# Kernel tuning notes

Hardware: AMD Instinct MI355X
Metric: run time of the kernel (lower is better)

Reference implementation:

```python
import jax, jax.numpy as jnp
import numpy as np

N_MOTIF_PER_CLASS = 8
N_CLASS = 16
N_MOTIF = N_MOTIF_PER_CLASS * N_CLASS
TEMPERATURE = 0.2
TAU = 0.99
K2 = 32
EPS = 1e-4


def setup_inputs() -> dict:
    key = jax.random.key(0)
    k1, k2, k3 = jax.random.split(key, 3)
    N, H = 32768, 1024
    z = jax.random.normal(k1, (N, H), dtype=jnp.float32)
    Motif_Vector = jax.random.normal(k2, (N_MOTIF, H), dtype=jnp.float32)
    y = jax.random.randint(k3, (N,), 0, N_CLASS, dtype=jnp.int64)
    return {"z": z, "Motif_Vector": Motif_Vector, "y": y}


def euclidean_1(X, M):
    # squared euclidean distance via GEMM, then log-ratio similarity
    xp = X @ M.T                                     # [N, n_motif]
    distance = (-2.0 * xp
                + jnp.sum(X * X, axis=1, keepdims=True)
                + jnp.sum(M * M, axis=1)[None, :])
    similarity = jnp.log((distance + 1.0) / (distance + EPS))
    return similarity, distance


def reference(z, Motif_Vector, y):
    similarity, distance = euclidean_1(z, Motif_Vector)

    # mapping: motif j belongs to class j // n_motif_per_class
    motif_class = jnp.arange(N_MOTIF) // N_MOTIF_PER_CLASS   # [n_motif]
    true_motifs = (y[:, None] == motif_class[None, :])       # [N, n_motif]

    # contrastive loss (exact torch math: exp(sim/T), max over positives,
    # sum over negatives)
    sims = jnp.exp(similarity / TEMPERATURE)
    sim_pos = jnp.max(jnp.where(true_motifs, sims, -jnp.inf), axis=1)
    sim_neg_sum = jnp.sum(jnp.where(true_motifs, 0.0, sims), axis=1)
    loss = -jnp.mean(jnp.log(sim_pos / (sim_neg_sum + sim_pos)))

    # update_motif (update_type='topk', weighted_mean=False):
    # torch passes `distance` into filter_similar_graph and argsorts
    # descending, i.e. selects the K2 LARGEST distances among same-class
    # samples (faithful to source).
    masked = jnp.where(true_motifs.T, distance.T, -jnp.inf)  # [n_motif, N]
    _, idx = jax.lax.top_k(masked, K2)                       # [n_motif, K2]
    selected = z[idx]                                        # [n_motif, K2, H]
    new_motif = jnp.mean(selected, axis=1)                   # weights = 1/K2
    new_M = TAU * Motif_Vector + (1.0 - TAU) * new_motif

    return loss, new_M
```

## Files before the change

kernel.cpp:

```cpp
#include <hip/hip_runtime.h>
#include <cstdint>
#include <cmath>

#define NROWS 32768
#define HD    1024
#define NMOT  128
#define NCLS  16
#define KSEL  32
#define EPSV  1e-4f

typedef __attribute__((ext_vector_type(4))) float  f32x4;
typedef __attribute__((ext_vector_type(8))) __bf16 bf16x8;
typedef __attribute__((ext_vector_type(4))) __bf16 bf16x4;
typedef unsigned long long u64;

#define WS_LP   0
#define WS_S1K  1024
#define WS_CD   132096
#define CAPC    256

static __device__ __forceinline__ float dot4(float4 v) {
    return v.x * v.x + v.y * v.y + v.z * v.z + v.w * v.w;
}

static __device__ __forceinline__ bf16x4 cvt4(float4 v) {
    bf16x4 t;
    t[0] = (__bf16)v.x; t[1] = (__bf16)v.y; t[2] = (__bf16)v.z; t[3] = (__bf16)v.w;
    return t;
}

static __device__ __forceinline__ bf16x8 cvt8(float4 a, float4 b) {
    bf16x8 t;
    t[0] = (__bf16)a.x; t[1] = (__bf16)a.y; t[2] = (__bf16)a.z; t[3] = (__bf16)a.w;
    t[4] = (__bf16)b.x; t[5] = (__bf16)b.y; t[6] = (__bf16)b.z; t[7] = (__bf16)b.w;
    return t;
}

static __device__ __forceinline__ u64 pack_key(float v, int idx) {
    unsigned int b = __float_as_uint(v);
    unsigned int mo = (b & 0x80000000u) ? ~b : (b | 0x80000000u);
    unsigned int khi = ~mo;
    return ((u64)khi << 32) | (unsigned int)idx;
}

#define BM 64
#define BN 128
#define BK 32
#define NS (HD / BK)
#define SA 40

__global__ __launch_bounds__(256, 2) void gemm_fused(
    const float* __restrict__ z, const float* __restrict__ mv,
    float* __restrict__ cd, const int* __restrict__ y,
    float* __restrict__ lossP) {
    __shared__ __bf16 As[2][BM * SA];
    __shared__ __bf16 Bs[2][BN * SA];
    __shared__ float  szn[BM];
    __shared__ float  smn[BN];
    __shared__ int    ly[BM];
    __shared__ float  spm[2][BM];
    __shared__ float  sns[2][BM];

    const int tid  = threadIdx.x;
    const int row0 = blockIdx.x * BM;
    const int lane = tid & 63;
    const int wave = tid >> 6;
    const int wr   = wave >> 1;
    const int wc   = wave & 1;
    const int l15  = lane & 15;
    const int quad = lane >> 4;

    const int sq = tid & 7;
    const int sr = tid >> 3;
    const int bq = tid & 3;
    const int br = tid >> 2;

    if (tid < BM) ly[tid] = y[row0 + tid];

    f32x4 acc[2][4];
#pragma unroll
    for (int i = 0; i < 2; ++i)
#pragma unroll
        for (int j = 0; j < 4; ++j) acc[i][j] = (f32x4){0.f, 0.f, 0.f, 0.f};

    float zsq0 = 0.f, zsq1 = 0.f;
    float msq0 = 0.f, msq1 = 0.f;

    const float* zb = z  + (size_t)(row0 + sr) * HD + sq * 4;
    const float* bb = mv + (size_t)br * HD + bq * 8;

    float4 ra0[4], ra1[4];
    float4 rb0[2][2], rb1[2][2];
#pragma unroll
    for (int s = 0; s < 4; ++s) {
        ra0[s] = *(const float4*)(zb + s * BK);
        ra1[s] = *(const float4*)(zb + s * BK + 32 * HD);
    }
#pragma unroll
    for (int s = 0; s < 2; ++s) {
        rb0[s][0] = *(const float4*)(bb + s * BK);
        rb0[s][1] = *(const float4*)(bb + s * BK + 4);
        rb1[s][0] = *(const float4*)(bb + s * BK + 64 * HD);
        rb1[s][1] = *(const float4*)(bb + s * BK + 64 * HD + 4);
    }
    *(bf16x4*)&As[0][sr * SA + sq * 4]        = cvt4(ra0[0]);
    *(bf16x4*)&As[0][(sr + 32) * SA + sq * 4] = cvt4(ra1[0]);
    *(bf16x8*)&Bs[0][br * SA + bq * 8]        = cvt8(rb0[0][0], rb0[0][1]);
    *(bf16x8*)&Bs[0][(br + 64) * SA + bq * 8] = cvt8(rb1[0][0], rb1[0][1]);
    zsq0 += dot4(ra0[0]); zsq1 += dot4(ra1[0]);
    msq0 += dot4(rb0[0][0]) + dot4(rb0[0][1]);
    msq1 += dot4(rb1[0][0]) + dot4(rb1[0][1]);
    ra0[0] = *(const float4*)(zb + 4 * BK);
    ra1[0] = *(const float4*)(zb + 4 * BK + 32 * HD);
    rb0[0][0] = *(const float4*)(bb + 2 * BK);
    rb0[0][1] = *(const float4*)(bb + 2 * BK + 4);
    rb1[0][0] = *(const float4*)(bb + 2 * BK + 64 * HD);
    rb1[0][1] = *(const float4*)(bb + 2 * BK + 64 * HD + 4);
    __syncthreads();

    for (int it = 0; it < NS / 4; ++it) {
#pragma unroll
        for (int u = 0; u < 4; ++u) {
            const int kt = it * 4 + u;
            const int rbuf = kt & 1;
            const int ko = quad * 8;
            bf16x8 af[2], bfr[4];
#pragma unroll
            for (int i = 0; i < 2; ++i)
                af[i] = *(const bf16x8*)&As[rbuf][(wr * 32 + i * 16 + l15) * SA + ko];
#pragma unroll
            for (int j = 0; j < 4; ++j)
                bfr[j] = *(const bf16x8*)&Bs[rbuf][(wc * 64 + j * 16 + l15) * SA + ko];
            if (kt + 1 < NS) {
                const int w  = (kt + 1) & 1;
                const int sA = (kt + 1) & 3;
                const int sB = (kt + 1) & 1;
                *(bf16x4*)&As[w][sr * SA + sq * 4]        = cvt4(ra0[sA]);
                *(bf16x4*)&As[w][(sr + 32) * SA + sq * 4] = cvt4(ra1[sA]);
                *(bf16x8*)&Bs[w][br * SA + bq * 8]        = cvt8(rb0[sB][0], rb0[sB][1]);
                *(bf16x8*)&Bs[w][(br + 64) * SA + bq * 8] = cvt8(rb1[sB][0], rb1[sB][1]);
                zsq0 += dot4(ra0[sA]); zsq1 += dot4(ra1[sA]);
                msq0 += dot4(rb0[sB][0]) + dot4(rb0[sB][1]);
                msq1 += dot4(rb1[sB][0]) + dot4(rb1[sB][1]);
                if (kt + 5 < NS) {
                    const float* zn = zb + (kt + 5) * BK;
                    ra0[sA] = *(const float4*)(zn);
                    ra1[sA] = *(const float4*)(zn + 32 * HD);
                }
                if (kt + 3 < NS) {
                    const float* bn = bb + (kt + 3) * BK;
                    rb0[sB][0] = *(const float4*)(bn);
                    rb0[sB][1] = *(const float4*)(bn + 4);
                    rb1[sB][0] = *(const float4*)(bn + 64 * HD);
                    rb1[sB][1] = *(const float4*)(bn + 64 * HD + 4);
                }
            }
#pragma unroll
            for (int i = 0; i < 2; ++i)
#pragma unroll
                for (int j = 0; j < 4; ++j)
                    acc[i][j] = __builtin_amdgcn_mfma_f32_16x16x32_bf16(
                        af[i], bfr[j], acc[i][j], 0, 0, 0);
            __syncthreads();
        }
    }

#pragma unroll
    for (int o = 1; o < 8; o <<= 1) {
        zsq0 += __shfl_xor(zsq0, o, 64);
        zsq1 += __shfl_xor(zsq1, o, 64);
    }
    if (sq == 0) { szn[sr] = zsq0; szn[sr + 32] = zsq1; }
#pragma unroll
    for (int o = 1; o < 4; o <<= 1) {
        msq0 += __shfl_xor(msq0, o, 64);
        msq1 += __shfl_xor(msq1, o, 64);
    }
    if (bq == 0) { smn[br] = msq0; smn[br + 64] = msq1; }
    __syncthreads();

    f32x4 znv[2];
    int rcls[2][4];
#pragma unroll
    for (int i = 0; i < 2; ++i) {
        znv[i] = *(const f32x4*)&szn[wr * 32 + i * 16 + quad * 4];
#pragma unroll
        for (int reg = 0; reg < 4; ++reg)
            rcls[i][reg] = ly[wr * 32 + i * 16 + quad * 4 + reg];
    }
    float pm[2][4], ns[2][4];
#pragma unroll
    for (int i = 0; i < 2; ++i)
#pragma unroll
        for (int reg = 0; reg < 4; ++reg) { pm[i][reg] = 0.f; ns[i][reg] = 0.f; }

#pragma unroll
    for (int j = 0; j < 4; ++j) {
        const int c = wc * 64 + j * 16 + l15;
        const float mc = smn[c];
        const int ccls = c >> 3;
#pragma unroll
        for (int i = 0; i < 2; ++i) {
#pragma unroll
            for (int reg = 0; reg < 4; ++reg) {
                const int row = wr * 32 + i * 16 + quad * 4 + reg;
                float d = znv[i][reg] + mc - 2.f * acc[i][j][reg];
                float r = (d + 1.0f) * __builtin_amdgcn_rcpf(d + EPSV);
                float r2 = r * r;
                float s = r2 * r2 * r;
                if (ccls == rcls[i][reg]) {
                    pm[i][reg] = fmaxf(pm[i][reg], s);
                    cd[(size_t)(row0 + row) * 8 + (c & 7)] = d;
                } else {
                    ns[i][reg] += s;
                }
            }
        }
    }
#pragma unroll
    for (int o = 1; o < 16; o <<= 1) {
#pragma unroll
        for (int i = 0; i < 2; ++i)
#pragma unroll
            for (int reg = 0; reg < 4; ++reg) {
                pm[i][reg] = fmaxf(pm[i][reg], __shfl_xor(pm[i][reg], o, 64));
                ns[i][reg] += __shfl_xor(ns[i][reg], o, 64);
            }
    }
    if (l15 == 0) {
#pragma unroll
        for (int i = 0; i < 2; ++i)
#pragma unroll
            for (int reg = 0; reg < 4; ++reg) {
                const int row = wr * 32 + i * 16 + quad * 4 + reg;
                spm[wc][row] = pm[i][reg];
                sns[wc][row] = ns[i][reg];
            }
    }
    __syncthreads();
    if (tid < BM) {
        float p = fmaxf(spm[0][tid], spm[1][tid]);
        float nsum = sns[0][tid] + sns[1][tid];
        float li = logf((nsum + p) / p);
#pragma unroll
        for (int o = 1; o < 64; o <<= 1) li += __shfl_xor(li, o, 64);
        if (tid == 0) lossP[blockIdx.x] = li;
    }
}

__global__ __launch_bounds__(256) void sel1_k(const int* __restrict__ y,
                                              const float* __restrict__ cd,
                                              u64* __restrict__ s1k) {
    __shared__ u64 keys[256];
    __shared__ int clist[CAPC];
    __shared__ int cnt;

    const int bid = blockIdx.x;
    const int j = bid >> 4, chunk = bid & 15;
    const int cls = j >> 3, m8 = j & 7;
    const int tid = threadIdx.x;
    const int lane = tid & 63;

    if (tid == 0) cnt = 0;
    __syncthreads();
    const int base = chunk * 2048;
#pragma unroll
    for (int t = 0; t < 8; ++t) {
        const int i = base + t * 256 + tid;
        const bool pred = (y[i] == cls);
        const u64 m = __ballot(pred);
        int wbase = 0;
        if (lane == 0 && m) wbase = atomicAdd(&cnt, (int)__popcll(m));
        wbase = __shfl(wbase, 0, 64);
        if (pred) {
            const int p = wbase + (int)__popcll(m & ((1ull << lane) - 1ull));
            if (p < CAPC) clist[p] = i;
        }
    }
    __syncthreads();
    const int n = cnt < CAPC ? cnt : CAPC;

    u64 key = ~0ull;
    if (tid < n) {
        const int idx = clist[tid];
        key = pack_key(cd[(size_t)idx * 8 + m8], idx);
    }
    keys[tid] = key;
    __syncthreads();

    for (int k = 2; k <= 256; k <<= 1) {
        for (int jj = k >> 1; jj > 0; jj >>= 1) {
            if (tid < 128) {
                const int i  = ((tid & ~(jj - 1)) << 1) | (tid & (jj - 1));
                const int ix = i | jj;
                const u64 A = keys[i], B = keys[ix];
                const bool up = ((i & k) == 0);
                if ((A > B) == up) { keys[i] = B; keys[ix] = A; }
            }
            __syncthreads();
        }
    }
    if (tid < KSEL) s1k[(size_t)j * 512 + chunk * KSEL + tid] = keys[tid];
}

__global__ __launch_bounds__(256) void merge_k(
    const float* __restrict__ z, const float* __restrict__ mv,
    const u64* __restrict__ s1k, const float* __restrict__ lossP,
    float* __restrict__ out) {
    __shared__ u64 keys[512];
    __shared__ int sel[KSEL];
    __shared__ float redf[4];

    const int b = blockIdx.x;
    const int j = b >> 2, q = b & 3;
    const int tid = threadIdx.x;
    const int lane = tid & 63;
    const int wave = tid >> 6;

    if (b == 0) {
        float s = lossP[tid] + lossP[tid + 256];
#pragma unroll
        for (int o = 1; o < 64; o <<= 1) s += __shfl_xor(s, o, 64);
        if (lane == 0) redf[wave] = s;
        __syncthreads();
        if (tid == 0)
            out[0] = (redf[0] + redf[1] + redf[2] + redf[3]) * (1.0f / NROWS);
    }

    keys[tid]       = s1k[(size_t)j * 512 + tid];
    keys[tid + 256] = s1k[(size_t)j * 512 + 256 + tid];
    __syncthreads();

    for (int k = 2; k <= 512; k <<= 1) {
        for (int jj = k >> 1; jj > 0; jj >>= 1) {
            const int i  = ((tid & ~(jj - 1)) << 1) | (tid & (jj - 1));
            const int ix = i | jj;
            const u64 A = keys[i], B = keys[ix];
            const bool up = ((i & k) == 0);
            if ((A > B) == up) { keys[i] = B; keys[ix] = A; }
            __syncthreads();
        }
    }
    if (tid < KSEL) sel[tid] = (int)(keys[tid] & 0xFFFFFFFFu);
    __syncthreads();

    const int h = q * 256 + tid;
    float s = 0.f;
#pragma unroll 8
    for (int r = 0; r < KSEL; ++r) s += z[(size_t)sel[r] * HD + h];
    out[1 + (size_t)j * HD + h] =
        0.99f * mv[(size_t)j * HD + h] + 0.01f * (s * (1.0f / KSEL));
}

extern "C" void kernel_launch(void* const* d_in, const int* in_sizes, int n_in,
                              void* d_out, int out_size, void* d_ws, size_t ws_size,
                              hipStream_t stream) {
    const float* z  = (const float*)d_in[0];
    const float* mv = (const float*)d_in[1];
    const int*   y  = (const int*)d_in[2];
    float* out = (float*)d_out;
    float* wsf = (float*)d_ws;
    float* lossP = wsf + WS_LP;
    u64*   s1k   = (u64*)(wsf + WS_S1K);
    float* cd    = wsf + WS_CD;

    hipLaunchKernelGGL(gemm_fused, dim3(NROWS / BM), dim3(256), 0, stream,
                       z, mv, cd, y, lossP);
    hipLaunchKernelGGL(sel1_k,     dim3(NMOT * 16), dim3(256), 0, stream,
                       y, cd, s1k);
    hipLaunchKernelGGL(merge_k,    dim3(NMOT * 4),  dim3(256), 0, stream,
                       z, mv, s1k, lossP, out);
}
```

Before: 229.7 us.

## Precompute bf16 motifs and norms; stream z directly to registers in GEMM

Adds a prep kernel that converts the motif matrix to bf16 and computes its squared norms once, instead of every GEMM block re-reading and converting the fp32 motifs. The GEMM now loads each wave's 16 z rows straight into registers as the A operand, skipping the LDS staging for A. B tiles are loaded with global_load_lds into a swizzled 4-deep LDS ring synchronised by explicit waitcnt and barriers. The cost is one extra launch and hand-tuned wait counts that must exactly match the number of outstanding loads.

```diff
diff --git a/kernel.cpp b/kernel.cpp
--- a/kernel.cpp
+++ b/kernel.cpp
@@ -15,8 +15,10 @@
 typedef unsigned long long u64;
 
 #define WS_LP   0
-#define WS_S1K  1024
-#define WS_CD   132096
+#define WS_MN   512
+#define WS_MVBF 1024
+#define WS_S1K  66560
+#define WS_CD   197632
 #define CAPC    256
 
 static __device__ __forceinline__ float dot4(float4 v) {
@@ -36,6 +38,12 @@
     return t;
 }
 
+static __device__ __forceinline__ void gl16(const void* g, void* l) {
+    __builtin_amdgcn_global_load_lds(
+        (const __attribute__((address_space(1))) void*)g,
+        (__attribute__((address_space(3))) void*)l, 16, 0, 0);
+}
+
 static __device__ __forceinline__ u64 pack_key(float v, int idx) {
     unsigned int b = __float_as_uint(v);
     unsigned int mo = (b & 0x80000000u) ? ~b : (b | 0x80000000u);
@@ -43,209 +51,169 @@
     return ((u64)khi << 32) | (unsigned int)idx;
 }
 
+__global__ __launch_bounds__(256) void prep_k(const float* __restrict__ mv,
+                                              float* __restrict__ mn,
+                                              __bf16* __restrict__ mvbf) {
+    const int b = blockIdx.x;
+    const int tid = threadIdx.x;
+    const int k = tid * 4;
+    float4 v = *(const float4*)&mv[(size_t)b * HD + k];
+    *(bf16x4*)&mvbf[(size_t)b * HD + k] = cvt4(v);
+    float s = dot4(v);
+#pragma unroll
+    for (int o = 1; o < 64; o <<= 1) s += __shfl_xor(s, o, 64);
+    __shared__ float red[4];
+    if ((tid & 63) == 0) red[tid >> 6] = s;
+    __syncthreads();
+    if (tid == 0) mn[b] = red[0] + red[1] + red[2] + red[3];
+}
+
 #define BM 64
-#define BN 128
 #define BK 32
 #define NS (HD / BK)
-#define SA 40
 
 __global__ __launch_bounds__(256, 2) void gemm_fused(
-    const float* __restrict__ z, const float* __restrict__ mv,
-    float* __restrict__ cd, const int* __restrict__ y,
-    float* __restrict__ lossP) {
-    __shared__ __bf16 As[2][BM * SA];
-    __shared__ __bf16 Bs[2][BN * SA];
-    __shared__ float  szn[BM];
-    __shared__ float  smn[BN];
-    __shared__ int    ly[BM];
-    __shared__ float  spm[2][BM];
-    __shared__ float  sns[2][BM];
+    const float* __restrict__ z, const __bf16* __restrict__ mvbf,
+    const float* __restrict__ mn, float* __restrict__ cd,
+    const int* __restrict__ y, float* __restrict__ lossP) {
+    __shared__ __align__(16) __bf16 Bs[4][4096];
+    __shared__ float redw[4];
 
     const int tid  = threadIdx.x;
-    const int row0 = blockIdx.x * BM;
     const int lane = tid & 63;
-    const int wave = tid >> 6;
-    const int wr   = wave >> 1;
-    const int wc   = wave & 1;
+    const int wid  = tid >> 6;
     const int l15  = lane & 15;
     const int quad = lane >> 4;
-
-    const int sq = tid & 7;
-    const int sr = tid >> 3;
-    const int bq = tid & 3;
-    const int br = tid >> 2;
-
-    if (tid < BM) ly[tid] = y[row0 + tid];
-
-    f32x4 acc[2][4];
-#pragma unroll
-    for (int i = 0; i < 2; ++i)
-#pragma unroll
-        for (int j = 0; j < 4; ++j) acc[i][j] = (f32x4){0.f, 0.f, 0.f, 0.f};
-
-    float zsq0 = 0.f, zsq1 = 0.f;
-    float msq0 = 0.f, msq1 = 0.f;
-
-    const float* zb = z  + (size_t)(row0 + sr) * HD + sq * 4;
-    const float* bb = mv + (size_t)br * HD + bq * 8;
-
-    float4 ra0[4], ra1[4];
-    float4 rb0[2][2], rb1[2][2];
-#pragma unroll
-    for (int s = 0; s < 4; ++s) {
-        ra0[s] = *(const float4*)(zb + s * BK);
-        ra1[s] = *(const float4*)(zb + s * BK + 32 * HD);
-    }
-#pragma unroll
-    for (int s = 0; s < 2; ++s) {
-        rb0[s][0] = *(const float4*)(bb + s * BK);
-        rb0[s][1] = *(const float4*)(bb + s * BK + 4);
-        rb1[s][0] = *(const float4*)(bb + s * BK + 64 * HD);
-        rb1[s][1] = *(const float4*)(bb + s * BK + 64 * HD + 4);
-    }
-    *(bf16x4*)&As[0][sr * SA + sq * 4]        = cvt4(ra0[0]);
-    *(bf16x4*)&As[0][(sr + 32) * SA + sq * 4] = cvt4(ra1[0]);
-    *(bf16x8*)&Bs[0][br * SA + bq * 8]        = cvt8(rb0[0][0], rb0[0][1]);
-    *(bf16x8*)&Bs[0][(br + 64) * SA + bq * 8] = cvt8(rb1[0][0], rb1[0][1]);
-    zsq0 += dot4(ra0[0]); zsq1 += dot4(ra1[0]);
-    msq0 += dot4(rb0[0][0]) + dot4(rb0[0][1]);
-    msq1 += dot4(rb1[0][0]) + dot4(rb1[0][1]);
-    ra0[0] = *(const float4*)(zb + 4 * BK);
-    ra1[0] = *(const float4*)(zb + 4 * BK + 32 * HD);
-    rb0[0][0] = *(const float4*)(bb + 2 * BK);
-    rb0[0][1] = *(const float4*)(bb + 2 * BK + 4);
-    rb1[0][0] = *(const float4*)(bb + 2 * BK + 64 * HD);
-    rb1[0][1] = *(const float4*)(bb + 2 * BK + 64 * HD + 4);
-    __syncthreads();
+    const int row0 = blockIdx.x * BM;
+    const int myrow = row0 + wid * 16 + l15;
+
+    const float* zrow = z + (size_t)myrow * HD + quad * 8;
+
+    const int g1 = tid, g2 = tid + 256;
+    const int r1 = g1 >> 2, r2 = g2 >> 2;
+    const int q1 = (g1 & 3) ^ ((r1 >> 1) & 3);
+    const int q2 = (g2 & 3) ^ ((r2 >> 1) & 3);
+    const __bf16* bsrc1 = mvbf + r1 * HD + q1 * 8;
+    const __bf16* bsrc2 = mvbf + r2 * HD + q2 * 8;
+    char* bs = (char*)Bs;
+    const int bofs = l15 * 64 + ((quad ^ ((l15 >> 1) & 3)) << 4);
+
+    float mcv[8];
+#pragma unroll
+    for (int j = 0; j < 8; ++j) mcv[j] = mn[j * 16 + l15];
+    const int yv = y[myrow];
+
+    f32x4 acc[8];
+#pragma unroll
+    for (int j = 0; j < 8; ++j) acc[j] = (f32x4){0.f, 0.f, 0.f, 0.f};
+    float zsq = 0.f;
+    float4 ra[2][2];
+
+    gl16(bsrc1,      bs + 0 * 8192 + wid * 1024);
+    gl16(bsrc2,      bs + 0 * 8192 + 4096 + wid * 1024);
+    gl16(bsrc1 + BK, bs + 1 * 8192 + wid * 1024);
+    gl16(bsrc2 + BK, bs + 1 * 8192 + 4096 + wid * 1024);
+    ra[0][0] = *(const float4*)(zrow);
+    ra[0][1] = *(const float4*)(zrow + 4);
+    ra[1][0] = *(const float4*)(zrow + BK);
+    ra[1][1] = *(const float4*)(zrow + BK + 4);
+    __builtin_amdgcn_sched_barrier(0);
+    asm volatile("s_waitcnt vmcnt(6)" ::: "memory");
+    __builtin_amdgcn_s_barrier();
+    asm volatile("" ::: "memory");
+    __builtin_amdgcn_sched_barrier(0);
 
     for (int it = 0; it < NS / 4; ++it) {
 #pragma unroll
         for (int u = 0; u < 4; ++u) {
             const int kt = it * 4 + u;
-            const int rbuf = kt & 1;
-            const int ko = quad * 8;
-            bf16x8 af[2], bfr[4];
-#pragma unroll
-            for (int i = 0; i < 2; ++i)
-                af[i] = *(const bf16x8*)&As[rbuf][(wr * 32 + i * 16 + l15) * SA + ko];
-#pragma unroll
-            for (int j = 0; j < 4; ++j)
-                bfr[j] = *(const bf16x8*)&Bs[rbuf][(wc * 64 + j * 16 + l15) * SA + ko];
-            if (kt + 1 < NS) {
-                const int w  = (kt + 1) & 1;
-                const int sA = (kt + 1) & 3;
-                const int sB = (kt + 1) & 1;
-                *(bf16x4*)&As[w][sr * SA + sq * 4]        = cvt4(ra0[sA]);
-                *(bf16x4*)&As[w][(sr + 32) * SA + sq * 4] = cvt4(ra1[sA]);
-                *(bf16x8*)&Bs[w][br * SA + bq * 8]        = cvt8(rb0[sB][0], rb0[sB][1]);
-                *(bf16x8*)&Bs[w][(br + 64) * SA + bq * 8] = cvt8(rb1[sB][0], rb1[sB][1]);
-                zsq0 += dot4(ra0[sA]); zsq1 += dot4(ra1[sA]);
-                msq0 += dot4(rb0[sB][0]) + dot4(rb0[sB][1]);
-                msq1 += dot4(rb1[sB][0]) + dot4(rb1[sB][1]);
-                if (kt + 5 < NS) {
-                    const float* zn = zb + (kt + 5) * BK;
-                    ra0[sA] = *(const float4*)(zn);
-                    ra1[sA] = *(const float4*)(zn + 32 * HD);
-                }
-                if (kt + 3 < NS) {
-                    const float* bn = bb + (kt + 3) * BK;
-                    rb0[sB][0] = *(const float4*)(bn);
-                    rb0[sB][1] = *(const float4*)(bn + 4);
-                    rb1[sB][0] = *(const float4*)(bn + 64 * HD);
-                    rb1[sB][1] = *(const float4*)(bn + 64 * HD + 4);
-                }
-            }
-#pragma unroll
-            for (int i = 0; i < 2; ++i)
-#pragma unroll
-                for (int j = 0; j < 4; ++j)
-                    acc[i][j] = __builtin_amdgcn_mfma_f32_16x16x32_bf16(
-                        af[i], bfr[j], acc[i][j], 0, 0, 0);
-            __syncthreads();
-        }
-    }
-
-#pragma unroll
-    for (int o = 1; o < 8; o <<= 1) {
-        zsq0 += __shfl_xor(zsq0, o, 64);
-        zsq1 += __shfl_xor(zsq1, o, 64);
-    }
-    if (sq == 0) { szn[sr] = zsq0; szn[sr + 32] = zsq1; }
-#pragma unroll
-    for (int o = 1; o < 4; o <<= 1) {
-        msq0 += __shfl_xor(msq0, o, 64);
-        msq1 += __shfl_xor(msq1, o, 64);
-    }
-    if (bq == 0) { smn[br] = msq0; smn[br + 64] = msq1; }
-    __syncthreads();
-
-    f32x4 znv[2];
-    int rcls[2][4];
-#pragma unroll
-    for (int i = 0; i < 2; ++i) {
-        znv[i] = *(const f32x4*)&szn[wr * 32 + i * 16 + quad * 4];
+            const int slot = u & 1;
+            bf16x8 bfr[8];
+#pragma unroll
+            for (int j = 0; j < 8; ++j)
+                bfr[j] = *(const bf16x8*)(bs + u * 8192 + j * 1024 + bofs);
+            if (kt + 2 < NS) {
+                char* d = bs + ((u + 2) & 3) * 8192 + wid * 1024;
+                gl16(bsrc1 + (kt + 2) * BK, d);
+                gl16(bsrc2 + (kt + 2) * BK, d + 4096);
+            }
+            bf16x8 af = cvt8(ra[slot][0], ra[slot][1]);
+            zsq += dot4(ra[slot][0]) + dot4(ra[slot][1]);
+            if (kt + 2 < NS) {
+                ra[slot][0] = *(const float4*)(zrow + (kt + 2) * BK);
+                ra[slot][1] = *(const float4*)(zrow + (kt + 2) * BK + 4);
+            }
+#pragma unroll
+            for (int j = 0; j < 8; ++j)
+                acc[j] = __builtin_amdgcn_mfma_f32_16x16x32_bf16(
+                    af, bfr[j], acc[j], 0, 0, 0);
+            if (kt + 2 < NS) {
+                __builtin_amdgcn_sched_barrier(0);
+                asm volatile("s_waitcnt vmcnt(4) lgkmcnt(0)" ::: "memory");
+                __builtin_amdgcn_s_barrier();
+                asm volatile("" ::: "memory");
+                __builtin_amdgcn_sched_barrier(0);
+            } else if (kt + 1 < NS) {
+                __builtin_amdgcn_sched_barrier(0);
+                asm volatile("s_waitcnt vmcnt(2) lgkmcnt(0)" ::: "memory");
+                __builtin_amdgcn_s_barrier();
+                asm volatile("" ::: "memory");
+                __builtin_amdgcn_sched_barrier(0);
+            }
+        }
+    }
+
+    zsq += __shfl_xor(zsq, 16, 64);
+    zsq += __shfl_xor(zsq, 32, 64);
+
+    float znv[4]; int rcls[4];
+#pragma unroll
+    for (int reg = 0; reg < 4; ++reg) {
+        znv[reg]  = __shfl(zsq, quad * 4 + reg, 64);
+        rcls[reg] = __shfl(yv,  quad * 4 + reg, 64);
+    }
+    float pm[4], ns[4];
+#pragma unroll
+    for (int reg = 0; reg < 4; ++reg) { pm[reg] = 0.f; ns[reg] = 0.f; }
+
+#pragma unroll
+    for (int j = 0; j < 8; ++j) {
+        const int c = j * 16 + l15;
+        const float mc = mcv[j];
+        const int ccls = c >> 3;
+#pragma unroll
+        for (int reg = 0; reg < 4; ++reg) {
+            float d = znv[reg] + mc - 2.f * acc[j][reg];
+            float r = (d + 1.0f) * __builtin_amdgcn_rcpf(d + EPSV);
+            float r2 = r * r;
+            float s = r2 * r2 * r;
+            if (ccls == rcls[reg]) {
+                pm[reg] = fmaxf(pm[reg], s);
+                const int row = row0 + wid * 16 + quad * 4 + reg;
+                cd[(size_t)row * 8 + (c & 7)] = d;
+            } else {
+                ns[reg] += s;
+            }
+        }
+    }
+#pragma unroll
+    for (int o = 1; o < 16; o <<= 1)
+#pragma unroll
+        for (int reg = 0; reg < 4; ++reg) {
+            pm[reg] = fmaxf(pm[reg], __shfl_xor(pm[reg], o, 64));
+            ns[reg] += __shfl_xor(ns[reg], o, 64);
+        }
+    float li = 0.f;
+    if (l15 == 0) {
 #pragma unroll
         for (int reg = 0; reg < 4; ++reg)
-            rcls[i][reg] = ly[wr * 32 + i * 16 + quad * 4 + reg];
-    }
-    float pm[2][4], ns[2][4];
-#pragma unroll
-    for (int i = 0; i < 2; ++i)
-#pragma unroll
-        for (int reg = 0; reg < 4; ++reg) { pm[i][reg] = 0.f; ns[i][reg] = 0.f; }
-
-#pragma unroll
-    for (int j = 0; j < 4; ++j) {
-        const int c = wc * 64 + j * 16 + l15;
-        const float mc = smn[c];
-        const int ccls = c >> 3;
-#pragma unroll
-        for (int i = 0; i < 2; ++i) {
-#pragma unroll
-            for (int reg = 0; reg < 4; ++reg) {
-                const int row = wr * 32 + i * 16 + quad * 4 + reg;
-                float d = znv[i][reg] + mc - 2.f * acc[i][j][reg];
-                float r = (d + 1.0f) * __builtin_amdgcn_rcpf(d + EPSV);
-                float r2 = r * r;
-                float s = r2 * r2 * r;
-                if (ccls == rcls[i][reg]) {
-                    pm[i][reg] = fmaxf(pm[i][reg], s);
-                    cd[(size_t)(row0 + row) * 8 + (c & 7)] = d;
-                } else {
-                    ns[i][reg] += s;
-                }
-            }
-        }
-    }
-#pragma unroll
-    for (int o = 1; o < 16; o <<= 1) {
-#pragma unroll
-        for (int i = 0; i < 2; ++i)
-#pragma unroll
-            for (int reg = 0; reg < 4; ++reg) {
-                pm[i][reg] = fmaxf(pm[i][reg], __shfl_xor(pm[i][reg], o, 64));
-                ns[i][reg] += __shfl_xor(ns[i][reg], o, 64);
-            }
-    }
-    if (l15 == 0) {
-#pragma unroll
-        for (int i = 0; i < 2; ++i)
-#pragma unroll
-            for (int reg = 0; reg < 4; ++reg) {
-                const int row = wr * 32 + i * 16 + quad * 4 + reg;
-                spm[wc][row] = pm[i][reg];
-                sns[wc][row] = ns[i][reg];
-            }
-    }
-    __syncthreads();
-    if (tid < BM) {
-        float p = fmaxf(spm[0][tid], spm[1][tid]);
-        float nsum = sns[0][tid] + sns[1][tid];
-        float li = logf((nsum + p) / p);
-#pragma unroll
-        for (int o = 1; o < 64; o <<= 1) li += __shfl_xor(li, o, 64);
-        if (tid == 0) lossP[blockIdx.x] = li;
-    }
+            li += logf((ns[reg] + pm[reg]) / pm[reg]);
+    }
+    li += __shfl_xor(li, 16, 64);
+    li += __shfl_xor(li, 32, 64);
+    if (lane == 0) redw[wid] = li;
+    __syncthreads();
+    if (tid == 0) lossP[blockIdx.x] = redw[0] + redw[1] + redw[2] + redw[3];
 }
 
 __global__ __launch_bounds__(256) void sel1_k(const int* __restrict__ y,
@@ -360,12 +328,16 @@
     const int*   y  = (const int*)d_in[2];
     float* out = (float*)d_out;
     float* wsf = (float*)d_ws;
-    float* lossP = wsf + WS_LP;
-    u64*   s1k   = (u64*)(wsf + WS_S1K);
-    float* cd    = wsf + WS_CD;
-
+    float*  lossP = wsf + WS_LP;
+    float*  mn    = wsf + WS_MN;
+    __bf16* mvbf  = (__bf16*)(wsf + WS_MVBF);
+    u64*    s1k   = (u64*)(wsf + WS_S1K);
+    float*  cd    = wsf + WS_CD;
+
+    hipLaunchKernelGGL(prep_k,     dim3(NMOT),      dim3(256), 0, stream,
+                       mv, mn, mvbf);
     hipLaunchKernelGGL(gemm_fused, dim3(NROWS / BM), dim3(256), 0, stream,
-                       z, mv, cd, y, lossP);
+                       z, mvbf, mn, cd, y, lossP);
     hipLaunchKernelGGL(sel1_k,     dim3(NMOT * 16), dim3(256), 0, stream,
                        y, cd, s1k);
     hipLaunchKernelGGL(merge_k,    dim3(NMOT * 4),  dim3(256), 0, stream,
```

After: 232.5 us. Within noise of the previous version (+1.2%).
